# Performance work log

Hardware: AMD Instinct MI355X
Metric: run time of the kernel (lower is better)

The kernel has to match this reference:

```python
import jax, jax.numpy as jnp
import numpy as np


def pairwise_distances(x):
    # x: [N, D] -> squared euclidean distances [N, N], clamped at 0
    sq = jnp.sum(x * x, axis=1)  # [N]
    dist = sq[:, None] + sq[None, :] - 2.0 * (x @ x.T)
    return jnp.maximum(dist, 0.0)


def setup_inputs() -> dict:
    key = jax.random.key(0)
    k1, k2 = jax.random.split(key)
    N, D, T = 8192, 128, 200000
    x = jax.random.normal(k1, (N, D), dtype=jnp.float32)
    triplets = jax.random.randint(k2, (T, 3), 0, N, dtype=jnp.int64)
    return {"x": x, "triplets": triplets}


def reference(x, triplets):
    dist = pairwise_distances(x)  # [N, N]
    i, j, k = triplets[:, 0], triplets[:, 1], triplets[:, 2]
    d_ij = dist[i, j]  # [T] anchor-positive distances
    d_ik = dist[i, k]  # [T] anchor-negative distances
    # loss = mean over triplets of log(1 + exp(d_ij - d_ik)) (uniform weights)
    loss = jnp.mean(jnp.log1p(jnp.exp(d_ij - d_ik)))
    return loss
```

## Files before the change

kernel.cpp:

```cpp
#include <hip/hip_runtime.h>
#include <math.h>

#define TRIP_BLOCKS 2048


template<int CTRL, int ROWMASK>
__device__ __forceinline__ float dpp_add(float v) {
    int m = __builtin_amdgcn_update_dpp(0, __float_as_int(v), CTRL, ROWMASK, 0xf, true);
    return v + __int_as_float(m);
}

__device__ __forceinline__ float wave64_sum(float v) {
    v = dpp_add<0x111, 0xf>(v);
    v = dpp_add<0x112, 0xf>(v);
    v = dpp_add<0x114, 0xf>(v);
    v = dpp_add<0x118, 0xf>(v);
    v = dpp_add<0x142, 0xa>(v);
    v = dpp_add<0x143, 0xc>(v);
    return v;
}

__device__ __forceinline__ float softplus_fast(float z) {
    float u = __expf(-fabsf(z));
    return fmaxf(z, 0.0f) + __logf(1.0f + u);
}

__global__ void __launch_bounds__(256)
trip_kernel(const float* __restrict__ x, const int* __restrict__ trip,
            float* __restrict__ partial, int T) {
    const int lane   = threadIdx.x & 63;
    const int wid    = threadIdx.x >> 6;
    const int gwave  = (blockIdx.x * blockDim.x + threadIdx.x) >> 6;
    const int nwaves = (TRIP_BLOCKS * 256) >> 6;

    const float2* xv = (const float2*)x;

    float local = 0.0f;

    int n = gwave;
    int i = 0, j = 0, k = 0;
    if (n < T) {
        int n0 = __builtin_amdgcn_readfirstlane(n);
        i = trip[3 * n0];
        j = trip[3 * n0 + 1];
        k = trip[3 * n0 + 2];
    }
    while (n < T) {
        float2 a = xv[(size_t)i * 64 + lane];
        float2 b = xv[(size_t)j * 64 + lane];
        float2 c = xv[(size_t)k * 64 + lane];

        int n2 = n + nwaves;
        if (n2 < T) {
            int n0 = __builtin_amdgcn_readfirstlane(n2);
            i = trip[3 * n0];
            j = trip[3 * n0 + 1];
            k = trip[3 * n0 + 2];
        }

        float t1 = a.x - b.x, t2 = a.x - c.x;
        float e  = t1 * t1;
        e = fmaf(-t2, t2, e);
        t1 = a.y - b.y; t2 = a.y - c.y;
        e = fmaf(t1, t1, e);
        e = fmaf(-t2, t2, e);

        e = wave64_sum(e);
        if (lane == 63)
            local += softplus_fast(e);
        n = n2;
    }

    __shared__ float wsum[4];
    if (lane == 63) wsum[wid] = local;
    __syncthreads();
    if (threadIdx.x == 0)
        partial[blockIdx.x] = wsum[0] + wsum[1] + wsum[2] + wsum[3];
}

__global__ void __launch_bounds__(256)
finalize_kernel(const float* __restrict__ partial, int nparts,
                float* __restrict__ out, int T) {
    float s = 0.0f;
    for (int idx = threadIdx.x; idx < nparts; idx += 256)
        s += partial[idx];
#pragma unroll
    for (int off = 32; off; off >>= 1) s += __shfl_xor(s, off, 64);
    __shared__ float wsum[4];
    int wid = threadIdx.x >> 6;
    if ((threadIdx.x & 63) == 0) wsum[wid] = s;
    __syncthreads();
    if (threadIdx.x == 0)
        out[0] = (wsum[0] + wsum[1] + wsum[2] + wsum[3]) / (float)T;
}

extern "C" void kernel_launch(void* const* d_in, const int* in_sizes, int n_in,
                              void* d_out, int out_size, void* d_ws, size_t ws_size,
                              hipStream_t stream) {
    const float* x    = (const float*)d_in[0];
    const int*   trip = (const int*)d_in[1];
    float*       out  = (float*)d_out;

    int T = in_sizes[1] / 3;

    float* partial = (float*)d_ws;

    trip_kernel<<<TRIP_BLOCKS, 256, 0, stream>>>(x, trip, partial, T);
    finalize_kernel<<<1, 256, 0, stream>>>(partial, TRIP_BLOCKS, out, T);
}
```

Baseline: 79.70 us.

## Split waves into half-wave triplet groups with float4 gathers and load prefetch

Each 64-lane wave now works on two triplets at once, one per 32-lane half. Each lane gathers float4 rows instead of float2, so the cross-lane reduction drops its final DPP step. The row loads for the next triplet are issued one iteration ahead, and the loop trip count is fixed and computed on the host, with out-of-range indices clamped and masked. The goal is more memory traffic in flight per wave and half as many serial iterations, to hide gather latency. The cost is more registers for the prefetched rows and some redundant clamped loads in the tail.

```diff
diff --git a/kernel.cpp b/kernel.cpp
--- a/kernel.cpp
+++ b/kernel.cpp
@@ -10,13 +10,12 @@
     return v + __int_as_float(m);
 }
 
-__device__ __forceinline__ float wave64_sum(float v) {
+__device__ __forceinline__ float half32_sum(float v) {
     v = dpp_add<0x111, 0xf>(v);
     v = dpp_add<0x112, 0xf>(v);
     v = dpp_add<0x114, 0xf>(v);
     v = dpp_add<0x118, 0xf>(v);
     v = dpp_add<0x142, 0xa>(v);
-    v = dpp_add<0x143, 0xc>(v);
     return v;
 }
 
@@ -27,52 +26,55 @@
 
 __global__ void __launch_bounds__(256)
 trip_kernel(const float* __restrict__ x, const int* __restrict__ trip,
-            float* __restrict__ partial, int T) {
-    const int lane   = threadIdx.x & 63;
-    const int wid    = threadIdx.x >> 6;
-    const int gwave  = (blockIdx.x * blockDim.x + threadIdx.x) >> 6;
-    const int nwaves = (TRIP_BLOCKS * 256) >> 6;
+            float* __restrict__ partial, int T, int iters) {
+    const int lane    = threadIdx.x & 63;
+    const int sub     = lane & 31;
+    const int gwave   = (blockIdx.x * blockDim.x + threadIdx.x) >> 6;
+    const int g0      = gwave * 2 + (lane >> 5);
+    const int ngroups = (TRIP_BLOCKS * 256) >> 5;
 
-    const float2* xv = (const float2*)x;
+    const float4* xv = (const float4*)x;
 
     float local = 0.0f;
 
-    int n = gwave;
-    int i = 0, j = 0, k = 0;
-    if (n < T) {
-        int n0 = __builtin_amdgcn_readfirstlane(n);
-        i = trip[3 * n0];
-        j = trip[3 * n0 + 1];
-        k = trip[3 * n0 + 2];
-    }
-    while (n < T) {
-        float2 a = xv[(size_t)i * 64 + lane];
-        float2 b = xv[(size_t)j * 64 + lane];
-        float2 c = xv[(size_t)k * 64 + lane];
+    int n  = g0;
+    int nc = n < T ? n : (T - 1);
+    int i0 = trip[3 * nc], j0 = trip[3 * nc + 1], k0 = trip[3 * nc + 2];
+    float4 A = xv[(size_t)i0 * 32 + sub];
+    float4 B = xv[(size_t)j0 * 32 + sub];
+    float4 C = xv[(size_t)k0 * 32 + sub];
+    int n1  = n + ngroups;
+    int nc1 = n1 < T ? n1 : (T - 1);
+    int i1 = trip[3 * nc1], j1 = trip[3 * nc1 + 1], k1 = trip[3 * nc1 + 2];
 
-        int n2 = n + nwaves;
-        if (n2 < T) {
-            int n0 = __builtin_amdgcn_readfirstlane(n2);
-            i = trip[3 * n0];
-            j = trip[3 * n0 + 1];
-            k = trip[3 * n0 + 2];
-        }
+#pragma unroll 2
+    for (int it = 0; it < iters; ++it) {
+        float4 nA = xv[(size_t)i1 * 32 + sub];
+        float4 nB = xv[(size_t)j1 * 32 + sub];
+        float4 nC = xv[(size_t)k1 * 32 + sub];
+        int n2  = n1 + ngroups;
+        int nc2 = n2 < T ? n2 : (T - 1);
+        int i2 = trip[3 * nc2], j2 = trip[3 * nc2 + 1], k2 = trip[3 * nc2 + 2];
 
-        float t1 = a.x - b.x, t2 = a.x - c.x;
-        float e  = t1 * t1;
-        e = fmaf(-t2, t2, e);
-        t1 = a.y - b.y; t2 = a.y - c.y;
-        e = fmaf(t1, t1, e);
-        e = fmaf(-t2, t2, e);
+        float t1, t2, e;
+        t1 = A.x - B.x; t2 = A.x - C.x; e = t1 * t1;      e = fmaf(-t2, t2, e);
+        t1 = A.y - B.y; t2 = A.y - C.y; e = fmaf(t1, t1, e); e = fmaf(-t2, t2, e);
+        t1 = A.z - B.z; t2 = A.z - C.z; e = fmaf(t1, t1, e); e = fmaf(-t2, t2, e);
+        t1 = A.w - B.w; t2 = A.w - C.w; e = fmaf(t1, t1, e); e = fmaf(-t2, t2, e);
 
-        e = wave64_sum(e);
-        if (lane == 63)
+        e = half32_sum(e);
+        if (sub == 31 && n < T)
             local += softplus_fast(e);
-        n = n2;
+
+        A = nA; B = nB; C = nC;
+        i1 = i2; j1 = j2; k1 = k2;
+        n = n1; n1 = n2;
     }
 
+    local += __shfl_xor(local, 32, 64);
     __shared__ float wsum[4];
-    if (lane == 63) wsum[wid] = local;
+    int wid = threadIdx.x >> 6;
+    if (lane == 31) wsum[wid] = local;
     __syncthreads();
     if (threadIdx.x == 0)
         partial[blockIdx.x] = wsum[0] + wsum[1] + wsum[2] + wsum[3];
@@ -103,8 +105,11 @@
 
     int T = in_sizes[1] / 3;
 
+    int ngroups = (TRIP_BLOCKS * 256) >> 5;
+    int iters   = (T + ngroups - 1) / ngroups;
+
     float* partial = (float*)d_ws;
 
-    trip_kernel<<<TRIP_BLOCKS, 256, 0, stream>>>(x, trip, partial, T);
+    trip_kernel<<<TRIP_BLOCKS, 256, 0, stream>>>(x, trip, partial, T, iters);
     finalize_kernel<<<1, 256, 0, stream>>>(partial, TRIP_BLOCKS, out, T);
 }
```

Result: faster. 76.97 us (-3.4%).

## Gather bf16 rows and compute triplet distances with MFMA using precomputed norms

Applied to the files above, without the earlier changes.

A new pre-pass converts x to bf16 and stores per-row squared norms in the workspace. The triplet kernel then handles 16 triplets per wave: it shuffles their indices across lanes, gathers bf16 fragments, and takes the i·j and i·k dot products from the diagonal of 16x16x32 bf16 MFMA products. Distances are rebuilt as sq_i + sq_j - 2·dot and clamped at zero, matching the reference formulation. This halves the bytes gathered per row and reduces per-triplet wave reductions, at the cost of bf16 rounding in the dot products, an extra kernel launch, and MFMA work of which only the diagonal is used.

```diff
diff --git a/kernel.cpp b/kernel.cpp
--- a/kernel.cpp
+++ b/kernel.cpp
@@ -1,7 +1,13 @@
 #include <hip/hip_runtime.h>
+#include <hip/hip_bf16.h>
 #include <math.h>
 
-#define TRIP_BLOCKS 2048
+#define TRIP_BLOCKS 1024
+#define N_ROWS 8192
+#define DIM 128
+
+using f32x4  = __attribute__((ext_vector_type(4))) float;
+using bf16x8 = __attribute__((ext_vector_type(8))) short;
 
 
 template<int CTRL, int ROWMASK>
@@ -9,7 +15,6 @@
     int m = __builtin_amdgcn_update_dpp(0, __float_as_int(v), CTRL, ROWMASK, 0xf, true);
     return v + __int_as_float(m);
 }
-
 __device__ __forceinline__ float wave64_sum(float v) {
     v = dpp_add<0x111, 0xf>(v);
     v = dpp_add<0x112, 0xf>(v);
@@ -26,51 +31,82 @@
 }
 
 __global__ void __launch_bounds__(256)
-trip_kernel(const float* __restrict__ x, const int* __restrict__ trip,
-            float* __restrict__ partial, int T) {
+cvt_kernel(const float* __restrict__ x, __hip_bfloat16* __restrict__ xh,
+           float* __restrict__ sq, int n_rows) {
+    int wave = (blockIdx.x * blockDim.x + threadIdx.x) >> 6;
+    int lane = threadIdx.x & 63;
+    if (wave >= n_rows) return;
+    const float2* row = (const float2*)(x + (size_t)wave * DIM);
+    float2 v = row[lane];
+    __hip_bfloat162 h = __float22bfloat162_rn(make_float2(v.x, v.y));
+    ((__hip_bfloat162*)xh)[wave * 64 + lane] = h;
+    float s = fmaf(v.x, v.x, v.y * v.y);
+    s = wave64_sum(s);
+    if (lane == 63) sq[wave] = s;
+}
+
+__global__ void __launch_bounds__(256)
+trip_kernel(const __hip_bfloat16* __restrict__ xh, const float* __restrict__ sq,
+            const int* __restrict__ trip, float* __restrict__ partial,
+            int T, int nbatches) {
     const int lane   = threadIdx.x & 63;
     const int wid    = threadIdx.x >> 6;
     const int gwave  = (blockIdx.x * blockDim.x + threadIdx.x) >> 6;
     const int nwaves = (TRIP_BLOCKS * 256) >> 6;
+    const int m      = lane & 15;
+    const int hi     = lane >> 4;
+    const bool isdiag = (hi == (m >> 2));
+    const int r      = m & 3;
 
-    const float2* xv = (const float2*)x;
+    const bf16x8* xq = (const bf16x8*)xh;
 
     float local = 0.0f;
 
-    int n = gwave;
-    int i = 0, j = 0, k = 0;
-    if (n < T) {
-        int n0 = __builtin_amdgcn_readfirstlane(n);
-        i = trip[3 * n0];
-        j = trip[3 * n0 + 1];
-        k = trip[3 * n0 + 2];
-    }
-    while (n < T) {
-        float2 a = xv[(size_t)i * 64 + lane];
-        float2 b = xv[(size_t)j * 64 + lane];
-        float2 c = xv[(size_t)k * 64 + lane];
+    int batch = gwave;
+    int idxv  = 0;
+    if (batch < nbatches && lane < 48)
+        idxv = trip[batch * 48 + lane];
 
-        int n2 = n + nwaves;
-        if (n2 < T) {
-            int n0 = __builtin_amdgcn_readfirstlane(n2);
-            i = trip[3 * n0];
-            j = trip[3 * n0 + 1];
-            k = trip[3 * n0 + 2];
+    while (batch < nbatches) {
+        int im = __shfl(idxv, 3 * m,     64);
+        int jm = __shfl(idxv, 3 * m + 1, 64);
+        int km = __shfl(idxv, 3 * m + 2, 64);
+
+        int ia = im * 16 + hi, ja = jm * 16 + hi, ka = km * 16 + hi;
+        bf16x8 fa0 = xq[ia], fa1 = xq[ia + 4], fa2 = xq[ia + 8], fa3 = xq[ia + 12];
+        bf16x8 fb0 = xq[ja], fb1 = xq[ja + 4], fb2 = xq[ja + 8], fb3 = xq[ja + 12];
+        bf16x8 fc0 = xq[ka], fc1 = xq[ka + 4], fc2 = xq[ka + 8], fc3 = xq[ka + 12];
+
+        float sqi = sq[im], sqj = sq[jm], sqk = sq[km];
+
+        int batch2 = batch + nwaves;
+        if (batch2 < nbatches && lane < 48)
+            idxv = trip[batch2 * 48 + lane];
+
+        f32x4 aij = {0.f, 0.f, 0.f, 0.f};
+        f32x4 aik = {0.f, 0.f, 0.f, 0.f};
+        aij = __builtin_amdgcn_mfma_f32_16x16x32_bf16(fa0, fb0, aij, 0, 0, 0);
+        aik = __builtin_amdgcn_mfma_f32_16x16x32_bf16(fa0, fc0, aik, 0, 0, 0);
+        aij = __builtin_amdgcn_mfma_f32_16x16x32_bf16(fa1, fb1, aij, 0, 0, 0);
+        aik = __builtin_amdgcn_mfma_f32_16x16x32_bf16(fa1, fc1, aik, 0, 0, 0);
+        aij = __builtin_amdgcn_mfma_f32_16x16x32_bf16(fa2, fb2, aij, 0, 0, 0);
+        aik = __builtin_amdgcn_mfma_f32_16x16x32_bf16(fa2, fc2, aik, 0, 0, 0);
+        aij = __builtin_amdgcn_mfma_f32_16x16x32_bf16(fa3, fb3, aij, 0, 0, 0);
+        aik = __builtin_amdgcn_mfma_f32_16x16x32_bf16(fa3, fc3, aik, 0, 0, 0);
+
+        if (isdiag && batch * 16 + m < T) {
+            float dij = (r & 2) ? ((r & 1) ? aij.w : aij.z)
+                                : ((r & 1) ? aij.y : aij.x);
+            float dik = (r & 2) ? ((r & 1) ? aik.w : aik.z)
+                                : ((r & 1) ? aik.y : aik.x);
+            float d1 = fmaxf(fmaf(-2.0f, dij, sqi + sqj), 0.0f);
+            float d2 = fmaxf(fmaf(-2.0f, dik, sqi + sqk), 0.0f);
+            local += softplus_fast(d1 - d2);
         }
-
-        float t1 = a.x - b.x, t2 = a.x - c.x;
-        float e  = t1 * t1;
-        e = fmaf(-t2, t2, e);
-        t1 = a.y - b.y; t2 = a.y - c.y;
-        e = fmaf(t1, t1, e);
-        e = fmaf(-t2, t2, e);
-
-        e = wave64_sum(e);
-        if (lane == 63)
-            local += softplus_fast(e);
-        n = n2;
+        batch = batch2;
     }
 
+    local = wave64_sum(local);
     __shared__ float wsum[4];
     if (lane == 63) wsum[wid] = local;
     __syncthreads();
@@ -101,10 +137,17 @@
     const int*   trip = (const int*)d_in[1];
     float*       out  = (float*)d_out;
 
-    int T = in_sizes[1] / 3;
+    int n_rows   = in_sizes[0] / DIM;
+    int T        = in_sizes[1] / 3;
+    int nbatches = (T + 15) / 16;
 
-    float* partial = (float*)d_ws;
+    __hip_bfloat16* xh = (__hip_bfloat16*)d_ws;
+    float* sq      = (float*)((char*)d_ws + (size_t)n_rows * DIM * 2);
+    float* partial = sq + n_rows;
 
-    trip_kernel<<<TRIP_BLOCKS, 256, 0, stream>>>(x, trip, partial, T);
+    cvt_kernel<<<(n_rows + 3) / 4, 256, 0, stream>>>(x, xh, sq, n_rows);
+
+    trip_kernel<<<TRIP_BLOCKS, 256, 0, stream>>>(xh, sq, trip, partial, T, nbatches);
+
     finalize_kernel<<<1, 256, 0, stream>>>(partial, TRIP_BLOCKS, out, T);
 }
```

After: 82.48 us. 1.03x slower.
